# Optimization experiments

Measured on AMD Instinct MI355X. Metric: run time of the kernel, lower is better.

The kernel has to match this reference:

```python
import jax, jax.numpy as jnp
import numpy as np

V = 50257   # vocab
P = 2048    # max positions
D = 768     # hidden
H = 12      # heads
F = 3072    # 4*D ffn
NL = 12     # layers
L = 2048    # seq len
EPS = 1e-5


def setup_inputs() -> dict:
    key = jax.random.key(0)
    ks = jax.random.split(key, 12)
    r = lambda k, shp: jax.random.normal(k, shp, jnp.float32) * 0.02
    return dict(
        input_ids=jax.random.randint(ks[0], (1, L), 0, V, dtype=jnp.int32),
        attention_mask=jnp.ones((1, L), jnp.int32),
        wte=r(ks[1], (V, D)),
        wpe=r(ks[2], (P, D)),
        lnf_w=jnp.ones((D,), jnp.float32),
        lnf_b=jnp.zeros((D,), jnp.float32),
        ln1_w=jnp.ones((NL, D), jnp.float32),
        ln1_b=jnp.zeros((NL, D), jnp.float32),
        qw=r(ks[3], (NL, D, D)),
        kw=r(ks[4], (NL, D, D)),
        vw=r(ks[5], (NL, D, D)),
        ow=r(ks[6], (NL, D, D)),
        ob=jnp.zeros((NL, D), jnp.float32),
        ln2_w=jnp.ones((NL, D), jnp.float32),
        ln2_b=jnp.zeros((NL, D), jnp.float32),
        fcw=r(ks[7], (NL, D, F)),
        fcb=jnp.zeros((NL, F), jnp.float32),
        pw=r(ks[8], (NL, F, D)),
        pb=jnp.zeros((NL, D), jnp.float32),
    )


def _ln(x, w, b):
    mu = jnp.mean(x, -1, keepdims=True)
    var = jnp.mean((x - mu) ** 2, -1, keepdims=True)
    return (x - mu) * jax.lax.rsqrt(var + EPS) * w + b


def reference(input_ids, attention_mask, wte, wpe, lnf_w, lnf_b,
              ln1_w, ln1_b, qw, kw, vw, ow, ob, ln2_w, ln2_b,
              fcw, fcb, pw, pb):
    ids = input_ids.reshape(-1, input_ids.shape[-1])          # [1, L]
    pos = jnp.cumsum(attention_mask, -1) - 1
    pos = jnp.where(attention_mask == 0, 1, pos)
    h = (wte[ids] + wpe[pos])[0]                               # [L, D]

    key_valid = attention_mask[0] > 0                          # actual_length mask
    mask = jnp.tril(jnp.ones((L, L), bool)) & key_valid[None, :]  # causal+pad
    dh = D // H

    def layer(h, p):
        l1w, l1b, Wq, Wk, Wv, Wo, bo, l2w, l2b, Wf, bf, Wp, bp = p
        x = _ln(h, l1w, l1b)
        q = (x @ Wq).reshape(L, H, dh)
        k = (x @ Wk).reshape(L, H, dh)
        v = (x @ Wv).reshape(L, H, dh)
        # GPT-Neo attention: NO 1/sqrt(dh) scaling
        scores = jnp.einsum('qhd,khd->hqk', q, k)
        scores = jnp.where(mask[None], scores, jnp.float32(-1e9))
        attn = jax.nn.softmax(scores, axis=-1)
        ctx = jnp.einsum('hqk,khd->qhd', attn, v).reshape(L, D)
        h = h + ctx @ Wo + bo
        y = _ln(h, l2w, l2b)
        h = h + jax.nn.gelu(y @ Wf + bf, approximate=True) @ Wp + bp
        return h, None

    h, _ = jax.lax.scan(layer, h, (ln1_w, ln1_b, qw, kw, vw, ow, ob,
                                   ln2_w, ln2_b, fcw, fcb, pw, pb))
    return _ln(h[None, :, :], lnf_w, lnf_b)                    # [1, L, D]
```

## Files before the change

### kernel.cpp

```cpp
#include <hip/hip_runtime.h>
#include <hip/hip_bf16.h>
#include <math.h>
#include <stdint.h>

#define L 2048
#define D 768
#define H 12
#define DH 64
#define F 3072
#define NL 12
#define QKVN 2304

typedef __attribute__((ext_vector_type(8))) short bf16x8;
typedef __attribute__((ext_vector_type(4))) float f32x4;

__device__ __forceinline__ ushort f2bf(float x) {
    union { float f; uint32_t u; } c; c.f = x;
    uint32_t r = c.u + 0x7FFFu + ((c.u >> 16) & 1u);
    return (ushort)(r >> 16);
}

__device__ __forceinline__ uint32_t cvt_pk_bf16(float lo, float hi) {
    uint32_t r;
    asm("v_cvt_pk_bf16_f32 %0, %1, %2" : "=v"(r) : "v"(lo), "v"(hi));
    return r;
}

__device__ __forceinline__ bf16x8 ldfrag(const ushort* p) {
    ushort4 lo = *(const ushort4*)(p);
    ushort4 hi = *(const ushort4*)(p + 16);
    bf16x8 f;
    f[0] = (short)lo.x; f[1] = (short)lo.y; f[2] = (short)lo.z; f[3] = (short)lo.w;
    f[4] = (short)hi.x; f[5] = (short)hi.y; f[6] = (short)hi.z; f[7] = (short)hi.w;
    return f;
}

__device__ __forceinline__ float gelu_tanh(float x) {
    float c = 0.7978845608028654f;
    float inner = c * (x + 0.044715f * x * x * x);
    return 0.5f * x * (1.0f + tanhf(inner));
}

__global__ void pos_kernel(const int* __restrict__ mask, int* __restrict__ pos) {
    __shared__ int sm[L];
    for (int i = threadIdx.x; i < L; i += blockDim.x) sm[i] = mask[i];
    __syncthreads();
    int t = blockIdx.x * blockDim.x + threadIdx.x;
    if (t < L) {
        int s = 0;
        for (int j = 0; j <= t; ++j) s += sm[j];
        int p = s - 1;
        if (sm[t] == 0) p = 1;
        pos[t] = p;
    }
}

__global__ void maskb_kernel(const int* __restrict__ mask, float* __restrict__ mb) {
    int i = blockIdx.x * blockDim.x + threadIdx.x;
    if (i < L) mb[i] = mask[i] ? 0.f : -1e9f;
}

__global__ __launch_bounds__(256) void embed_kernel(const int* __restrict__ ids,
                                                    const int* __restrict__ pos,
                                                    const float* __restrict__ wte,
                                                    const float* __restrict__ wpe,
                                                    float* __restrict__ h) {
    int t = blockIdx.x;
    int id = ids[t];
    int p = pos[t];
    const float* we = wte + (size_t)id * D;
    const float* wp = wpe + (size_t)p * D;
    float* hr = h + (size_t)t * D;
#pragma unroll
    for (int i = 0; i < 3; ++i) {
        int d = threadIdx.x + i * 256;
        hr[d] = we[d] + wp[d];
    }
}

template <bool OUTBF>
__global__ __launch_bounds__(256) void ln_kernel(const float* __restrict__ in,
                                                 const float* __restrict__ w,
                                                 const float* __restrict__ b,
                                                 float* __restrict__ outF,
                                                 ushort* __restrict__ outB) {
    __shared__ float red[2][4];
    int row = blockIdx.x;
    const float* x = in + (size_t)row * D;
    int t = threadIdx.x;
    float v0 = x[t], v1 = x[t + 256], v2 = x[t + 512];
    float s = v0 + v1 + v2;
    float ss = v0 * v0 + v1 * v1 + v2 * v2;
#pragma unroll
    for (int o = 32; o; o >>= 1) {
        s += __shfl_xor(s, o);
        ss += __shfl_xor(ss, o);
    }
    int wave = t >> 6;
    if ((t & 63) == 0) { red[0][wave] = s; red[1][wave] = ss; }
    __syncthreads();
    s = red[0][0] + red[0][1] + red[0][2] + red[0][3];
    ss = red[1][0] + red[1][1] + red[1][2] + red[1][3];
    float mean = s * (1.f / D);
    float var = ss * (1.f / D) - mean * mean;
    float rstd = rsqrtf(var + 1e-5f);
#pragma unroll
    for (int i = 0; i < 3; ++i) {
        int d = t + i * 256;
        float vv = (i == 0) ? v0 : (i == 1) ? v1 : v2;
        float y = (vv - mean) * rstd * w[d] + b[d];
        if (OUTBF) outB[(size_t)row * D + d] = f2bf(y);
        else       outF[(size_t)row * D + d] = y;
    }
}

template <int S, bool OUTBF>
__global__ __launch_bounds__(256) void redln_kernel(const float* __restrict__ part,
                                                    const float* __restrict__ bias,
                                                    float* __restrict__ h,
                                                    const float* __restrict__ lnw,
                                                    const float* __restrict__ lnb,
                                                    ushort* __restrict__ outB,
                                                    float* __restrict__ outF) {
    __shared__ float red[2][4];
    int row = blockIdx.x;
    int t = threadIdx.x;
    float v[3];
    float s = 0.f, ss = 0.f;
#pragma unroll
    for (int i = 0; i < 3; ++i) {
        int d = t + i * 256;
        float x = h[(size_t)row * D + d] + bias[d];
#pragma unroll
        for (int sp = 0; sp < S; ++sp)
            x += part[((size_t)sp * L + row) * D + d];
        v[i] = x;
        h[(size_t)row * D + d] = x;
        s += x;
        ss += x * x;
    }
#pragma unroll
    for (int o = 32; o; o >>= 1) {
        s += __shfl_xor(s, o);
        ss += __shfl_xor(ss, o);
    }
    int wave = t >> 6;
    if ((t & 63) == 0) { red[0][wave] = s; red[1][wave] = ss; }
    __syncthreads();
    s = red[0][0] + red[0][1] + red[0][2] + red[0][3];
    ss = red[1][0] + red[1][1] + red[1][2] + red[1][3];
    float mean = s * (1.f / D);
    float var = ss * (1.f / D) - mean * mean;
    float rstd = rsqrtf(var + 1e-5f);
#pragma unroll
    for (int i = 0; i < 3; ++i) {
        int d = t + i * 256;
        float y = (v[i] - mean) * rstd * lnw[d] + lnb[d];
        if (OUTBF) outB[(size_t)row * D + d] = f2bf(y);
        else       outF[(size_t)row * D + d] = y;
    }
}

__global__ __launch_bounds__(256) void tcast_f32(const float* __restrict__ in,
                                                 ushort* __restrict__ out,
                                                 int K, int N,
                                                 size_t inStride, size_t outStride) {
    in += blockIdx.z * inStride;
    out += blockIdx.z * outStride;
    __shared__ float tile[64][65];
    int k0 = blockIdx.y * 64, n0 = blockIdx.x * 64;
    int t = threadIdx.x;
    int cl = t & 63, rg = t >> 6;
#pragma unroll
    for (int i = 0; i < 16; ++i) {
        int r = rg + 4 * i;
        tile[r][cl] = in[(size_t)(k0 + r) * N + n0 + cl];
    }
    __syncthreads();
#pragma unroll
    for (int i = 0; i < 16; ++i) {
        int r = rg + 4 * i;
        out[(size_t)(n0 + r) * K + k0 + cl] = f2bf(tile[cl][r]);
    }
}

template <int ACT, bool OUTBF, int SPLITK, bool VSPLIT>
__global__ __launch_bounds__(256) void gemm_bf16(const ushort* __restrict__ A,
                                                 const ushort* __restrict__ Bt,
                                                 const float* __restrict__ bias,
                                                 const float* __restrict__ resid,
                                                 float* __restrict__ outF,
                                                 ushort* __restrict__ outB,
                                                 float* __restrict__ pout,
                                                 ushort* __restrict__ vTout,
                                                 int M, int N, int K) {
    __shared__ __align__(16) char lds[32768];
    const int tid = threadIdx.x;
    const int lane = tid & 63, w = tid >> 6;
    const int wr = w >> 1, wc = w & 1;
    const int bm = blockIdx.y * 128, bn = blockIdx.x * 128;
    const int l15 = lane & 15, l4 = lane >> 4;
    const int srow = tid >> 2, c = tid & 3;
    const int blo = (c & 1) * 32 + (c >> 1) * 8;
    const int kLen = K / SPLITK;
    const int kStart = (SPLITK > 1) ? blockIdx.z * kLen : 0;

    const int sxor = (srow & 3) << 4;
    const int wo0 = srow * 64 + (blo ^ sxor);
    const int wo1 = srow * 64 + ((blo + 16) ^ sxor);
    const int rxor = (l4 * 16) ^ ((l15 & 3) << 4);
    const int aBase = (wr * 64 + l15) * 64 + rxor;
    const int bBase = (wc * 64 + l15) * 64 + rxor;

    f32x4 acc[4][4];
#pragma unroll
    for (int m = 0; m < 4; ++m)
#pragma unroll
        for (int n = 0; n < 4; ++n)
            acc[m][n] = (f32x4){0.f, 0.f, 0.f, 0.f};

    const ushort* Ag = A + (size_t)(bm + srow) * K + kStart + c * 8;
    const ushort* Ag2 = Ag + (size_t)64 * K;
    const ushort* Bg = Bt + (size_t)(bn + srow) * K + kStart + c * 8;
    const ushort* Bg2 = Bg + (size_t)64 * K;

    uint4 a0 = *(const uint4*)(Ag);
    uint4 a1 = *(const uint4*)(Ag2);
    uint4 b0 = *(const uint4*)(Bg);
    uint4 b1 = *(const uint4*)(Bg2);

    for (int k0 = 0; k0 < kLen; k0 += 32) {
        char* Ab = lds + ((k0 >> 5) & 1) * 16384;
        char* Bb = Ab + 8192;
        uint2 t0, t1;
        t0.x = a0.x; t0.y = a0.y; t1.x = a0.z; t1.y = a0.w;
        *(uint2*)(Ab + wo0) = t0;
        *(uint2*)(Ab + wo1) = t1;
        t0.x = a1.x; t0.y = a1.y; t1.x = a1.z; t1.y = a1.w;
        *(uint2*)(Ab + wo0 + 4096) = t0;
        *(uint2*)(Ab + wo1 + 4096) = t1;
        t0.x = b0.x; t0.y = b0.y; t1.x = b0.z; t1.y = b0.w;
        *(uint2*)(Bb + wo0) = t0;
        *(uint2*)(Bb + wo1) = t1;
        t0.x = b1.x; t0.y = b1.y; t1.x = b1.z; t1.y = b1.w;
        *(uint2*)(Bb + wo0 + 4096) = t0;
        *(uint2*)(Bb + wo1 + 4096) = t1;
        __syncthreads();
        if (k0 + 32 < kLen) {
            a0 = *(const uint4*)(Ag + k0 + 32);
            a1 = *(const uint4*)(Ag2 + k0 + 32);
            b0 = *(const uint4*)(Bg + k0 + 32);
            b1 = *(const uint4*)(Bg2 + k0 + 32);
        }
        bf16x8 af[4], bfv[4];
#pragma unroll
        for (int m = 0; m < 4; ++m)
            af[m] = *(const bf16x8*)(Ab + aBase + m * 1024);
#pragma unroll
        for (int n = 0; n < 4; ++n)
            bfv[n] = *(const bf16x8*)(Bb + bBase + n * 1024);
#pragma unroll
        for (int m = 0; m < 4; ++m)
#pragma unroll
            for (int n = 0; n < 4; ++n)
                acc[m][n] = __builtin_amdgcn_mfma_f32_16x16x32_bf16(af[m], bfv[n], acc[m][n], 0, 0, 0);
    }

    if (SPLITK > 1) {
        const size_t sb = (size_t)blockIdx.z * M;
#pragma unroll
        for (int m = 0; m < 4; ++m)
#pragma unroll
            for (int n = 0; n < 4; ++n) {
                int col = bn + wc * 64 + n * 16 + l15;
#pragma unroll
                for (int r = 0; r < 4; ++r) {
                    int row = bm + wr * 64 + m * 16 + l4 * 4 + r;
                    pout[(sb + row) * N + col] = acc[m][n][r];
                }
            }
    } else {
#pragma unroll
        for (int m = 0; m < 4; ++m)
#pragma unroll
            for (int n = 0; n < 4; ++n) {
                int col = bn + wc * 64 + n * 16 + l15;
                int row0 = bm + wr * 64 + m * 16 + l4 * 4;
                if (VSPLIT && col >= 2 * D) {
                    ushort4 pk;
                    pk.x = f2bf(acc[m][n][0]);
                    pk.y = f2bf(acc[m][n][1]);
                    pk.z = f2bf(acc[m][n][2]);
                    pk.w = f2bf(acc[m][n][3]);
                    *(ushort4*)(vTout + (size_t)(col - 2 * D) * L + row0) = pk;
                } else {
#pragma unroll
                    for (int r = 0; r < 4; ++r) {
                        int row = row0 + r;
                        float v = acc[m][n][r];
                        if (bias) v += bias[col];
                        if (ACT == 1) v = gelu_tanh(v);
                        if (resid) v += resid[(size_t)row * N + col];
                        if (OUTBF) outB[(size_t)row * N + col] = f2bf(v);
                        else       outF[(size_t)row * N + col] = v;
                    }
                }
            }
    }
}

template <int NS>
__global__ __launch_bounds__(256) void attn_kernel(const ushort* __restrict__ qkv,
                                                   const ushort* __restrict__ vT,
                                                   const float* __restrict__ maskb,
                                                   float* __restrict__ po,
                                                   float* __restrict__ pm,
                                                   float* __restrict__ pl) {
    __shared__ __align__(16) char Kl[2][8192];
    __shared__ __align__(16) char Vl[2][8192];
    __shared__ float Ml[2][64];
    const int hh = blockIdx.y;
    const int sp = blockIdx.z;
    const int q0 = ((int)gridDim.x - 1 - (int)blockIdx.x) * 64;
    const int tid = threadIdx.x;
    const int lane = tid & 63, w = tid >> 6;
    const int l15 = lane & 15, l4 = lane >> 4;
    const int qg = q0 + w * 16 + l15;
    const int qmin = q0 + w * 16;

    const int nt = q0 / 64 + 1;
    const int chunk = (nt + NS - 1) / NS;
    const int it0 = sp * chunk;
    int it1 = it0 + chunk;
    if (it1 > nt) it1 = nt;

    f32x4 o[4];
#pragma unroll
    for (int i = 0; i < 4; ++i) o[i] = (f32x4){0.f, 0.f, 0.f, 0.f};
    float mrun = -1e30f, lrun = 0.f;

    if (it0 < it1) {
        bf16x8 qf[2];
#pragma unroll
        for (int ks = 0; ks < 2; ++ks)
            qf[ks] = ldfrag(qkv + (size_t)qg * QKVN + hh * 64 + ks * 32 + l4 * 4);

        const int srow = tid >> 2, c = tid & 3;
        const int blo = (c & 1) * 32 + (c >> 1) * 8;
        const int swz = (srow & 7) << 4;
        const int rb = srow * 128;
        const int lo4 = blo & 15;
        const int s0 = rb + (((blo)      & 0x70) ^ swz) + lo4;
        const int s1 = rb + (((blo + 16) & 0x70) ^ swz) + lo4;
        const int s2 = rb + (((blo + 64) & 0x70) ^ swz) + lo4;
        const int s3 = rb + (((blo + 80) & 0x70) ^ swz) + lo4;
        const int fxor = (l15 & 7) << 4;

        const ushort* Ksrc = qkv + (size_t)srow * QKVN + D + hh * 64 + c * 8;
        const ushort* Vsrc = vT + (size_t)(hh * 64 + srow) * L + c * 8;

        uint4 ka, kb, va, vb;
        float mv = 0.f;
        {
            const size_t koff = (size_t)(it0 * 64) * QKVN;
            ka = *(const uint4*)(Ksrc + koff);
            kb = *(const uint4*)(Ksrc + koff + 32);
            va = *(const uint4*)(Vsrc + it0 * 64);
            vb = *(const uint4*)(Vsrc + it0 * 64 + 32);
            if (tid < 64) mv = maskb[it0 * 64 + tid];
        }

        for (int it = it0; it < it1; ++it) {
            const int kv0 = it * 64;
            const int b = it & 1;
            {
                char* Kb = Kl[b];
                char* Vb = Vl[b];
                uint2 t0, t1;
                t0.x = ka.x; t0.y = ka.y; t1.x = ka.z; t1.y = ka.w;
                *(uint2*)(Kb + s0) = t0;
                *(uint2*)(Kb + s1) = t1;
                t0.x = kb.x; t0.y = kb.y; t1.x = kb.z; t1.y = kb.w;
                *(uint2*)(Kb + s2) = t0;
                *(uint2*)(Kb + s3) = t1;
                t0.x = va.x; t0.y = va.y; t1.x = va.z; t1.y = va.w;
                *(uint2*)(Vb + s0) = t0;
                *(uint2*)(Vb + s1) = t1;
                t0.x = vb.x; t0.y = vb.y; t1.x = vb.z; t1.y = vb.w;
                *(uint2*)(Vb + s2) = t0;
                *(uint2*)(Vb + s3) = t1;
                if (tid < 64) Ml[b][tid] = mv;
            }
            __syncthreads();
            if (it + 1 < it1) {
                const size_t koff = (size_t)(kv0 + 64) * QKVN;
                ka = *(const uint4*)(Ksrc + koff);
                kb = *(const uint4*)(Ksrc + koff + 32);
                va = *(const uint4*)(Vsrc + kv0 + 64);
                vb = *(const uint4*)(Vsrc + kv0 + 96);
                if (tid < 64) mv = maskb[kv0 + 64 + tid];
            }

            const char* Kb = Kl[b];
            const char* Vb = Vl[b];

            f32x4 st[4];
#pragma unroll
            for (int m = 0; m < 4; ++m) st[m] = (f32x4){0.f, 0.f, 0.f, 0.f};
#pragma unroll
            for (int m = 0; m < 4; ++m)
#pragma unroll
                for (int ks = 0; ks < 2; ++ks) {
                    bf16x8 kf = *(const bf16x8*)(Kb + (m * 16 + l15) * 128 +
                                                 ((ks * 64 + l4 * 16) ^ fxor));
                    st[m] = __builtin_amdgcn_mfma_f32_16x16x32_bf16(kf, qf[ks], st[m], 0, 0, 0);
                }

            float p[4][4];
            float tmax = -1e30f;
            const bool full = (kv0 + 63 <= qmin);
            if (full) {
#pragma unroll
                for (int m = 0; m < 4; ++m)
#pragma unroll
                    for (int r = 0; r < 4; ++r) {
                        int kl = m * 16 + l4 * 4 + r;
                        float s = st[m][r] + Ml[b][kl];
                        p[m][r] = s;
                        tmax = fmaxf(tmax, s);
                    }
            } else {
#pragma unroll
                for (int m = 0; m < 4; ++m)
#pragma unroll
                    for (int r = 0; r < 4; ++r) {
                        int kl = m * 16 + l4 * 4 + r;
                        float s = st[m][r] + Ml[b][kl];
                        if (kv0 + kl > qg) s = -1e30f;
                        p[m][r] = s;
                        tmax = fmaxf(tmax, s);
                    }
            }
            tmax = fmaxf(tmax, __shfl_xor(tmax, 16));
            tmax = fmaxf(tmax, __shfl_xor(tmax, 32));
            const bool noresc = __all(tmax <= mrun);
            float mnew = noresc ? mrun : fmaxf(mrun, tmax);
            float scale = noresc ? 1.f : __expf(mrun - mnew);
            float ts = 0.f;
#pragma unroll
            for (int m = 0; m < 4; ++m)
#pragma unroll
                for (int r = 0; r < 4; ++r) {
                    float e = __expf(p[m][r] - mnew);
                    p[m][r] = e;
                    ts += e;
                }
            ts += __shfl_xor(ts, 16);
            ts += __shfl_xor(ts, 32);
            lrun = lrun * scale + ts;
            mrun = mnew;

            bf16x8 pf[2];
#pragma unroll
            for (int g = 0; g < 2; ++g) {
                union { bf16x8 v; uint32_t d[4]; } pu;
                pu.d[0] = cvt_pk_bf16(p[2 * g][0], p[2 * g][1]);
                pu.d[1] = cvt_pk_bf16(p[2 * g][2], p[2 * g][3]);
                pu.d[2] = cvt_pk_bf16(p[2 * g + 1][0], p[2 * g + 1][1]);
                pu.d[3] = cvt_pk_bf16(p[2 * g + 1][2], p[2 * g + 1][3]);
                pf[g] = pu.v;
            }
            if (!noresc) {
#pragma unroll
                for (int i = 0; i < 4; ++i) {
                    o[i][0] *= scale; o[i][1] *= scale; o[i][2] *= scale; o[i][3] *= scale;
                }
            }
#pragma unroll
            for (int dhb = 0; dhb < 4; ++dhb)
#pragma unroll
                for (int g = 0; g < 2; ++g) {
                    bf16x8 vf = *(const bf16x8*)(Vb + (dhb * 16 + l15) * 128 +
                                                 ((g * 64 + l4 * 16) ^ fxor));
                    o[dhb] = __builtin_amdgcn_mfma_f32_16x16x32_bf16(vf, pf[g], o[dhb], 0, 0, 0);
                }
        }
    }

    const size_t pb = (size_t)(sp * H + hh) * L + qg;
    if (l4 == 0) { pm[pb] = mrun; pl[pb] = lrun; }
    float* op = po + pb * 64;
#pragma unroll
    for (int dhb = 0; dhb < 4; ++dhb)
        *(f32x4*)(op + dhb * 16 + l4 * 4) = o[dhb];
}

template <int NS>
__global__ __launch_bounds__(256) void attn_combine(const float* __restrict__ po,
                                                    const float* __restrict__ pm,
                                                    const float* __restrict__ pl,
                                                    ushort* __restrict__ ctx) {
    const int hh = blockIdx.y;
    const int q = blockIdx.x * 64 + (threadIdx.x >> 2);
    const int d0 = (threadIdx.x & 3) * 16;
    size_t idx[NS];
    float mm = -1e30f;
#pragma unroll
    for (int s = 0; s < NS; ++s) {
        idx[s] = (size_t)(s * H + hh) * L + q;
        mm = fmaxf(mm, pm[idx[s]]);
    }
    float e[NS];
    float l = 0.f;
#pragma unroll
    for (int s = 0; s < NS; ++s) {
        e[s] = __expf(pm[idx[s]] - mm);
        l += pl[idx[s]] * e[s];
    }
    float rinv = 1.0f / l;
    ushort* cp = ctx + (size_t)q * D + hh * 64 + d0;
#pragma unroll
    for (int j = 0; j < 16; j += 4) {
        float acc[4] = {0.f, 0.f, 0.f, 0.f};
#pragma unroll
        for (int s = 0; s < NS; ++s) {
            const float* op = po + idx[s] * 64 + d0 + j;
            float4 v = *(const float4*)op;
            acc[0] += v.x * e[s];
            acc[1] += v.y * e[s];
            acc[2] += v.z * e[s];
            acc[3] += v.w * e[s];
        }
        ushort4 pk;
        pk.x = f2bf(acc[0] * rinv);
        pk.y = f2bf(acc[1] * rinv);
        pk.z = f2bf(acc[2] * rinv);
        pk.w = f2bf(acc[3] * rinv);
        *(ushort4*)(cp + j) = pk;
    }
}

extern "C" void kernel_launch(void* const* d_in, const int* in_sizes, int n_in,
                              void* d_out, int out_size, void* d_ws, size_t ws_size,
                              hipStream_t stream) {
    const int* ids = (const int*)d_in[0];
    const int* amask = (const int*)d_in[1];
    const float* wte = (const float*)d_in[2];
    const float* wpe = (const float*)d_in[3];
    const float* lnf_w = (const float*)d_in[4];
    const float* lnf_b = (const float*)d_in[5];
    const float* ln1_w = (const float*)d_in[6];
    const float* ln1_b = (const float*)d_in[7];
    const float* qw = (const float*)d_in[8];
    const float* kw = (const float*)d_in[9];
    const float* vw = (const float*)d_in[10];
    const float* ow = (const float*)d_in[11];
    const float* ob = (const float*)d_in[12];
    const float* ln2_w = (const float*)d_in[13];
    const float* ln2_b = (const float*)d_in[14];
    const float* fcw = (const float*)d_in[15];
    const float* fcb = (const float*)d_in[16];
    const float* pw = (const float*)d_in[17];
    const float* pb = (const float*)d_in[18];

    char* p = (char*)d_ws;
    auto take = [&](size_t bytes) -> char* {
        char* r = p;
        p += (bytes + 4095) & ~(size_t)4095;
        return r;
    };
    ushort* wqkvT = (ushort*)take((size_t)NL * QKVN * D * 2);
    ushort* woT   = (ushort*)take((size_t)NL * D * D * 2);
    ushort* fcwT  = (ushort*)take((size_t)NL * F * D * 2);
    ushort* pwT   = (ushort*)take((size_t)NL * D * F * 2);
    float*  h     = (float*)take((size_t)L * D * 4);
    ushort* xb    = (ushort*)take((size_t)L * D * 2);
    ushort* qkvb  = (ushort*)take((size_t)L * QKVN * 2);
    ushort* vTb   = (ushort*)take((size_t)D * L * 2);
    ushort* ctxb  = (ushort*)take((size_t)L * D * 2);
    ushort* f1b   = (ushort*)take((size_t)L * F * 2);
    float*  pk    = (float*)take((size_t)4 * L * D * 4);
    float*  po    = (float*)take((size_t)2 * H * L * 64 * 4);
    float*  pm    = (float*)take((size_t)2 * H * L * 4);
    float*  pl    = (float*)take((size_t)2 * H * L * 4);
    float*  mb    = (float*)take(L * 4);
    int*    pos   = (int*)take(L * 4);

    pos_kernel<<<8, 256, 0, stream>>>(amask, pos);
    maskb_kernel<<<8, 256, 0, stream>>>(amask, mb);
    embed_kernel<<<L, 256, 0, stream>>>(ids, pos, wte, wpe, h);

    tcast_f32<<<dim3(12, 12, NL), 256, 0, stream>>>(qw, wqkvT, D, D,
                                                    (size_t)D * D, (size_t)QKVN * D);
    tcast_f32<<<dim3(12, 12, NL), 256, 0, stream>>>(kw, wqkvT + (size_t)D * D, D, D,
                                                    (size_t)D * D, (size_t)QKVN * D);
    tcast_f32<<<dim3(12, 12, NL), 256, 0, stream>>>(vw, wqkvT + (size_t)2 * D * D, D, D,
                                                    (size_t)D * D, (size_t)QKVN * D);
    tcast_f32<<<dim3(12, 12, NL), 256, 0, stream>>>(ow, woT, D, D,
                                                    (size_t)D * D, (size_t)D * D);
    tcast_f32<<<dim3(48, 12, NL), 256, 0, stream>>>(fcw, fcwT, D, F,
                                                    (size_t)D * F, (size_t)F * D);
    tcast_f32<<<dim3(12, 48, NL), 256, 0, stream>>>(pw, pwT, F, D,
                                                    (size_t)F * D, (size_t)D * F);

    ln_kernel<true><<<L, 256, 0, stream>>>(h, ln1_w, ln1_b, nullptr, xb);

    for (int l = 0; l < NL; ++l) {
        gemm_bf16<0, true, 1, true><<<dim3(QKVN / 128, L / 128), 256, 0, stream>>>(
            xb, wqkvT + (size_t)l * QKVN * D, nullptr, nullptr, nullptr, qkvb, nullptr,
            vTb, L, QKVN, D);
        attn_kernel<2><<<dim3(L / 64, H, 2), 256, 0, stream>>>(qkvb, vTb, mb,
                                                               po, pm, pl);
        attn_combine<2><<<dim3(L / 64, H), 256, 0, stream>>>(po, pm, pl, ctxb);
        gemm_bf16<0, true, 4, false><<<dim3(D / 128, L / 128, 4), 256, 0, stream>>>(
            ctxb, woT + (size_t)l * D * D, nullptr, nullptr, nullptr, nullptr, pk,
            nullptr, L, D, D);
        redln_kernel<4, true><<<L, 256, 0, stream>>>(
            pk, ob + l * D, h, ln2_w + l * D, ln2_b + l * D, xb, nullptr);
        gemm_bf16<1, true, 1, false><<<dim3(F / 128, L / 128), 256, 0, stream>>>(
            xb, fcwT + (size_t)l * F * D, fcb + l * F, nullptr, nullptr, f1b, nullptr,
            nullptr, L, F, D);
        gemm_bf16<0, true, 4, false><<<dim3(D / 128, L / 128, 4), 256, 0, stream>>>(
            f1b, pwT + (size_t)l * D * F, nullptr, nullptr, nullptr, nullptr, pk,
            nullptr, L, D, F);
        if (l < NL - 1) {
            redln_kernel<4, true><<<L, 256, 0, stream>>>(
                pk, pb + l * D, h, ln1_w + (l + 1) * D, ln1_b + (l + 1) * D, xb, nullptr);
        } else {
            redln_kernel<4, false><<<L, 256, 0, stream>>>(
                pk, pb + l * D, h, lnf_w, lnf_b, nullptr, (float*)d_out);
        }
    }
}
```

Baseline: 1.825 ms.

## Deepen GEMM K-tile to 64 and switch attention softmax to native exp2

The bf16 GEMM now stages 64-wide K tiles (doubling LDS to 64KB with a new 8-row XOR swizzle) and issues two MFMAs per fragment pair per iteration, halving the number of barriers and loop iterations. Separately, attention scores are pre-scaled by log2(e) and exponentials use the hardware v_exp_f32 instruction directly instead of __expf, removing a multiply per exponential. The mask bias is changed to -2e9 to keep masked keys equivalent after the base change. The larger LDS footprint may reduce occupancy for the GEMM.

```diff
diff --git a/kernel.cpp b/kernel.cpp
--- a/kernel.cpp
+++ b/kernel.cpp
@@ -25,6 +25,14 @@
     asm("v_cvt_pk_bf16_f32 %0, %1, %2" : "=v"(r) : "v"(lo), "v"(hi));
     return r;
 }
+
+__device__ __forceinline__ float ex2(float x) {
+    float r;
+    asm("v_exp_f32 %0, %1" : "=v"(r) : "v"(x));
+    return r;
+}
+
+#define LOG2E 1.4426950408889634f
 
 __device__ __forceinline__ bf16x8 ldfrag(const ushort* p) {
     ushort4 lo = *(const ushort4*)(p);
@@ -57,7 +65,7 @@
 
 __global__ void maskb_kernel(const int* __restrict__ mask, float* __restrict__ mb) {
     int i = blockIdx.x * blockDim.x + threadIdx.x;
-    if (i < L) mb[i] = mask[i] ? 0.f : -1e9f;
+    if (i < L) mb[i] = mask[i] ? 0.f : -2.0e9f;
 }
 
 __global__ __launch_bounds__(256) void embed_kernel(const int* __restrict__ ids,
@@ -194,23 +202,27 @@
                                                  float* __restrict__ pout,
                                                  ushort* __restrict__ vTout,
                                                  int M, int N, int K) {
-    __shared__ __align__(16) char lds[32768];
+    __shared__ __align__(16) char lds[65536];
     const int tid = threadIdx.x;
     const int lane = tid & 63, w = tid >> 6;
     const int wr = w >> 1, wc = w & 1;
     const int bm = blockIdx.y * 128, bn = blockIdx.x * 128;
     const int l15 = lane & 15, l4 = lane >> 4;
-    const int srow = tid >> 2, c = tid & 3;
-    const int blo = (c & 1) * 32 + (c >> 1) * 8;
     const int kLen = K / SPLITK;
     const int kStart = (SPLITK > 1) ? blockIdx.z * kLen : 0;
 
-    const int sxor = (srow & 3) << 4;
-    const int wo0 = srow * 64 + (blo ^ sxor);
-    const int wo1 = srow * 64 + ((blo + 16) ^ sxor);
-    const int rxor = (l4 * 16) ^ ((l15 & 3) << 4);
-    const int aBase = (wr * 64 + l15) * 64 + rxor;
-    const int bBase = (wc * 64 + l15) * 64 + rxor;
+    const int srow = tid >> 1, hf = tid & 1;
+    const int swz = (srow & 7) << 4;
+    const int rb = srow * 128;
+    int offlo[4], offhi[4];
+#pragma unroll
+    for (int cc = 0; cc < 4; ++cc) {
+        int blo = (cc & 1) * 32 + ((cc >> 1) & 1) * 8 + hf * 64;
+        offlo[cc] = rb + ((blo & 0x70) ^ swz) + (blo & 15);
+        int bhi = blo + 16;
+        offhi[cc] = rb + ((bhi & 0x70) ^ swz) + (bhi & 15);
+    }
+    const int fxor = (l15 & 7) << 4;
 
     f32x4 acc[4][4];
 #pragma unroll
@@ -219,51 +231,61 @@
         for (int n = 0; n < 4; ++n)
             acc[m][n] = (f32x4){0.f, 0.f, 0.f, 0.f};
 
-    const ushort* Ag = A + (size_t)(bm + srow) * K + kStart + c * 8;
-    const ushort* Ag2 = Ag + (size_t)64 * K;
-    const ushort* Bg = Bt + (size_t)(bn + srow) * K + kStart + c * 8;
-    const ushort* Bg2 = Bg + (size_t)64 * K;
-
-    uint4 a0 = *(const uint4*)(Ag);
-    uint4 a1 = *(const uint4*)(Ag2);
-    uint4 b0 = *(const uint4*)(Bg);
-    uint4 b1 = *(const uint4*)(Bg2);
-
-    for (int k0 = 0; k0 < kLen; k0 += 32) {
-        char* Ab = lds + ((k0 >> 5) & 1) * 16384;
-        char* Bb = Ab + 8192;
-        uint2 t0, t1;
-        t0.x = a0.x; t0.y = a0.y; t1.x = a0.z; t1.y = a0.w;
-        *(uint2*)(Ab + wo0) = t0;
-        *(uint2*)(Ab + wo1) = t1;
-        t0.x = a1.x; t0.y = a1.y; t1.x = a1.z; t1.y = a1.w;
-        *(uint2*)(Ab + wo0 + 4096) = t0;
-        *(uint2*)(Ab + wo1 + 4096) = t1;
-        t0.x = b0.x; t0.y = b0.y; t1.x = b0.z; t1.y = b0.w;
-        *(uint2*)(Bb + wo0) = t0;
-        *(uint2*)(Bb + wo1) = t1;
-        t0.x = b1.x; t0.y = b1.y; t1.x = b1.z; t1.y = b1.w;
-        *(uint2*)(Bb + wo0 + 4096) = t0;
-        *(uint2*)(Bb + wo1 + 4096) = t1;
+    const ushort* Ag = A + (size_t)(bm + srow) * K + kStart + hf * 32;
+    const ushort* Bg = Bt + (size_t)(bn + srow) * K + kStart + hf * 32;
+
+    uint4 ax[4], bx[4];
+#pragma unroll
+    for (int cc = 0; cc < 4; ++cc) {
+        ax[cc] = *(const uint4*)(Ag + cc * 8);
+        bx[cc] = *(const uint4*)(Bg + cc * 8);
+    }
+
+    for (int k0 = 0; k0 < kLen; k0 += 64) {
+        char* Ab = lds + ((k0 >> 6) & 1) * 32768;
+        char* Bb = Ab + 16384;
+        {
+            uint2 t0, t1;
+#pragma unroll
+            for (int cc = 0; cc < 4; ++cc) {
+                t0.x = ax[cc].x; t0.y = ax[cc].y; t1.x = ax[cc].z; t1.y = ax[cc].w;
+                *(uint2*)(Ab + offlo[cc]) = t0;
+                *(uint2*)(Ab + offhi[cc]) = t1;
+                t0.x = bx[cc].x; t0.y = bx[cc].y; t1.x = bx[cc].z; t1.y = bx[cc].w;
+                *(uint2*)(Bb + offlo[cc]) = t0;
+                *(uint2*)(Bb + offhi[cc]) = t1;
+            }
+        }
         __syncthreads();
-        if (k0 + 32 < kLen) {
-            a0 = *(const uint4*)(Ag + k0 + 32);
-            a1 = *(const uint4*)(Ag2 + k0 + 32);
-            b0 = *(const uint4*)(Bg + k0 + 32);
-            b1 = *(const uint4*)(Bg2 + k0 + 32);
+        if (k0 + 64 < kLen) {
+#pragma unroll
+            for (int cc = 0; cc < 4; ++cc) {
+                ax[cc] = *(const uint4*)(Ag + k0 + 64 + cc * 8);
+                bx[cc] = *(const uint4*)(Bg + k0 + 64 + cc * 8);
+            }
         }
-        bf16x8 af[4], bfv[4];
+        bf16x8 af[4][2], bfv[4][2];
 #pragma unroll
         for (int m = 0; m < 4; ++m)
-            af[m] = *(const bf16x8*)(Ab + aBase + m * 1024);
+#pragma unroll
+            for (int ks = 0; ks < 2; ++ks)
+                af[m][ks] = *(const bf16x8*)(Ab + (wr * 64 + m * 16 + l15) * 128 +
+                                             ((ks * 64 + l4 * 16) ^ fxor));
 #pragma unroll
         for (int n = 0; n < 4; ++n)
-            bfv[n] = *(const bf16x8*)(Bb + bBase + n * 1024);
+#pragma unroll
+            for (int ks = 0; ks < 2; ++ks)
+                bfv[n][ks] = *(const bf16x8*)(Bb + (wc * 64 + n * 16 + l15) * 128 +
+                                              ((ks * 64 + l4 * 16) ^ fxor));
 #pragma unroll
         for (int m = 0; m < 4; ++m)
 #pragma unroll
-            for (int n = 0; n < 4; ++n)
-                acc[m][n] = __builtin_amdgcn_mfma_f32_16x16x32_bf16(af[m], bfv[n], acc[m][n], 0, 0, 0);
+            for (int n = 0; n < 4; ++n) {
+                acc[m][n] = __builtin_amdgcn_mfma_f32_16x16x32_bf16(
+                    af[m][0], bfv[n][0], acc[m][n], 0, 0, 0);
+                acc[m][n] = __builtin_amdgcn_mfma_f32_16x16x32_bf16(
+                    af[m][1], bfv[n][1], acc[m][n], 0, 0, 0);
+            }
     }
 
     if (SPLITK > 1) {
@@ -425,7 +447,7 @@
 #pragma unroll
                     for (int r = 0; r < 4; ++r) {
                         int kl = m * 16 + l4 * 4 + r;
-                        float s = st[m][r] + Ml[b][kl];
+                        float s = fmaf(st[m][r], LOG2E, Ml[b][kl]);
                         p[m][r] = s;
                         tmax = fmaxf(tmax, s);
                     }
@@ -435,7 +457,7 @@
 #pragma unroll
                     for (int r = 0; r < 4; ++r) {
                         int kl = m * 16 + l4 * 4 + r;
-                        float s = st[m][r] + Ml[b][kl];
+                        float s = fmaf(st[m][r], LOG2E, Ml[b][kl]);
                         if (kv0 + kl > qg) s = -1e30f;
                         p[m][r] = s;
                         tmax = fmaxf(tmax, s);
@@ -445,13 +467,13 @@
             tmax = fmaxf(tmax, __shfl_xor(tmax, 32));
             const bool noresc = __all(tmax <= mrun);
             float mnew = noresc ? mrun : fmaxf(mrun, tmax);
-            float scale = noresc ? 1.f : __expf(mrun - mnew);
+            float scale = noresc ? 1.f : ex2(mrun - mnew);
             float ts = 0.f;
 #pragma unroll
             for (int m = 0; m < 4; ++m)
 #pragma unroll
                 for (int r = 0; r < 4; ++r) {
-                    float e = __expf(p[m][r] - mnew);
+                    float e = ex2(p[m][r] - mnew);
                     p[m][r] = e;
                     ts += e;
                 }
@@ -514,7 +536,7 @@
     float l = 0.f;
 #pragma unroll
     for (int s = 0; s < NS; ++s) {
-        e[s] = __expf(pm[idx[s]] - mm);
+        e[s] = ex2(pm[idx[s]] - mm);
         l += pl[idx[s]] * e[s];
     }
     float rinv = 1.0f / l;
```

Result: faster. 1.777 ms (-2.6%).
